# Kernel optimization log

Hardware: AMD Instinct MI355X
Metric: run time of the kernel (lower is better)

The kernel has to match this reference:

```python
import jax, jax.numpy as jnp
import numpy as np

VOCAB, EMBD, H1, H2, OUT = 100000, 128, 256, 128, 1
EPS = 1e-12

def _layernorm(x, g, b):
    mu = jnp.mean(x, axis=-1, keepdims=True)
    var = jnp.mean(jnp.square(x - mu), axis=-1, keepdims=True)
    return (x - mu) * jax.lax.rsqrt(var + EPS) * g + b

def setup_inputs() -> dict:
    key = jax.random.key(0)
    ks = jax.random.split(key, 10)
    B, S = 4096, 50
    return {
        "entity_ids": jax.random.randint(ks[0], (B, S), 0, VOCAB),
        "entity_length": jax.random.randint(ks[1], (B,), 0, S + 1),
        "emb_table": jax.random.normal(ks[2], (VOCAB, EMBD), jnp.float32),
        "ln1_g": jnp.ones((EMBD,), jnp.float32),
        "ln1_b": jnp.zeros((EMBD,), jnp.float32),
        "w1": jax.random.normal(ks[3], (EMBD, H1), jnp.float32) * (1.0 / np.sqrt(EMBD)),
        "b1": jnp.zeros((H1,), jnp.float32),
        "w2": jax.random.normal(ks[4], (H1, H2), jnp.float32) * (1.0 / np.sqrt(H1)),
        "b2": jnp.zeros((H2,), jnp.float32),
        "ln2_g": jnp.ones((H2,), jnp.float32),
        "ln2_b": jnp.zeros((H2,), jnp.float32),
        "fc_w": jax.random.normal(ks[5], (H2, OUT), jnp.float32) * (1.0 / np.sqrt(H2)),
        "fc_b": jnp.zeros((OUT,), jnp.float32),
    }

def reference(entity_ids, entity_length, emb_table, ln1_g, ln1_b, w1, b1, w2, b2, ln2_g, ln2_b, fc_w, fc_b):
    # embed: [B, S, EMBD]
    x = emb_table[entity_ids]
    x = _layernorm(x, ln1_g, ln1_b)
    # MLP (dropout is identity in eval); torch GELU default is exact erf form
    x = jax.nn.gelu(x @ w1 + b1, approximate=False) @ w2 + b2  # [B, S, H2]
    # ragged max-pool over first length positions (length 0 treated as 1)
    lengths = jnp.maximum(entity_length, 1)  # [B]
    S = x.shape[1]
    mask = jnp.arange(S)[None, :] < lengths[:, None]  # [B, S]
    x = jnp.max(jnp.where(mask[:, :, None], x, -jnp.inf), axis=1)  # [B, H2]
    x = _layernorm(x, ln2_g, ln2_b)
    return (x @ fc_w + fc_b).squeeze(-1)  # [B]
```

## Files before the change

kernel.cpp:

```cpp
#include <hip/hip_runtime.h>
#include <hip/hip_bf16.h>
#include <math.h>

typedef __attribute__((ext_vector_type(8))) _Float16 half8;
typedef __attribute__((ext_vector_type(4))) _Float16 half4;
typedef __attribute__((ext_vector_type(4))) float f32x4;

#define EMBD 128
#define H1 256
#define H2 128
#define SLEN 50
#define NROWS 4096
#define MTILE 32
#define DENSE_GRID 256

#define WS_FRAGS   0
#define WS_CNT     131072
#define WS_PACKED  131200
#define WS_PARTIAL 950400

__device__ __forceinline__ float gelu_exact(float h) {
    float ah = fabsf(h);
    float d  = fmaf(0.23163845f, ah, 1.0f);
    float t;
    asm("v_rcp_f32 %0, %1" : "=v"(t) : "v"(d));
    float p = fmaf(1.061405429f, t, -1.453152027f);
    p = fmaf(p, t, 1.421413741f);
    p = fmaf(p, t, -0.284496736f);
    p = fmaf(p, t, 0.254829592f);
    p = p * t;
    float e;
    float x2 = h * h * -0.72134752f;
    asm("v_exp_f32 %0, %1" : "=v"(e) : "v"(x2));
    float er = fmaf(-p, e, 1.0f);
    return fmaf(0.5f * ah, er, 0.5f * h);
}

#define BARRIER_LDS() asm volatile("s_waitcnt lgkmcnt(0)\n\ts_barrier" ::: "memory")

__global__ __launch_bounds__(256) void prep_kernel(
    const float* __restrict__ w1, const float* __restrict__ w2,
    half8* __restrict__ frags, int* __restrict__ cnt,
    float* __restrict__ partial)
{
    int b = blockIdx.x, t = threadIdx.x;
    if (b < 32) {
        int f = b * 256 + t;
        half8 v;
        if (f < 4096) {
            int fragid = f >> 6, lane = f & 63;
            int kt = fragid >> 4, nt = fragid & 15;
            int col = nt * 16 + (lane & 15);
            int kb  = kt * 32 + (lane >> 4) * 8;
            #pragma unroll
            for (int i = 0; i < 8; ++i) v[i] = (_Float16)w1[(size_t)(kb + i) * H1 + col];
            frags[f] = v;
        } else {
            int f2 = f - 4096;
            int fragid = f2 >> 6, lane = f2 & 63;
            int kt = fragid >> 3, ntc = fragid & 7;
            int col = ntc * 16 + (lane & 15);
            int kb  = kt * 32 + (lane >> 4) * 8;
            #pragma unroll
            for (int i = 0; i < 8; ++i) v[i] = (_Float16)w2[(size_t)(kb + i) * H2 + col];
            frags[4096 + f2] = v;
        }
    } else if (b == 32) {
        if (t == 0) *cnt = 0;
    } else {
        int idx = (b - 33) * 256 + t;
        if (idx < NROWS * 256) {
            int r = idx >> 8, rem = idx & 255;
            partial[(size_t)r * 384 + 128 + rem] = -INFINITY;
        }
    }
}

__global__ __launch_bounds__(256) void compact_kernel(
    const int* __restrict__ ids, const int* __restrict__ lens,
    unsigned* __restrict__ packed, int* __restrict__ cnt)
{
    int gtid = blockIdx.x * 256 + threadIdx.x;
    int lane = threadIdx.x & 63;
    int len = lens[gtid]; len = len < 1 ? 1 : (len > SLEN ? SLEN : len);
    int inc = len;
    #pragma unroll
    for (int off = 1; off < 64; off <<= 1) {
        int v = __shfl_up(inc, off, 64);
        if (lane >= off) inc += v;
    }
    int wave_total = __shfl(inc, 63, 64);
    int wbase;
    if (lane == 0) wbase = atomicAdd(cnt, wave_total);
    wbase = __shfl(wbase, 0, 64);
    int base = wbase + inc - len;
    unsigned rtag = (unsigned)gtid << 17;
    for (int t = 0; t < len; ++t)
        packed[base + t] = (unsigned)ids[gtid * SLEN + t] | rtag;
}

__global__ __launch_bounds__(512) void dense_kernel(
    const unsigned* __restrict__ packed, const int* __restrict__ cnt,
    const float* __restrict__ emb, const float* __restrict__ ln1g,
    const float* __restrict__ ln1b, const float* __restrict__ b1,
    const float* __restrict__ b2, const half8* __restrict__ wfrag,
    float* __restrict__ partial)
{
    const int tid = threadIdx.x;
    const int w  = tid >> 6;
    const int l  = tid & 63;
    const int ln = l & 15;
    const int lg = l >> 4;
    const int g32 = w * 4 + lg;

    __shared__ __align__(16) half8 wlds[8192];
    __shared__ __align__(16) _Float16 x_lds[MTILE][EMBD + 8];
    __shared__ __align__(16) _Float16 h1_lds[MTILE][H1 + 8];
    __shared__ unsigned tok_lds[MTILE + 1];

    #pragma unroll
    for (int i = 0; i < 16; ++i)
        wlds[i * 512 + tid] = wfrag[i * 512 + tid];

    float g1r[8], b1r[8];
    #pragma unroll
    for (int i = 0; i < 8; ++i) { g1r[i] = ln1g[ln * 8 + i]; b1r[i] = ln1b[ln * 8 + i]; }
    f32x4 b1tv[2];
    #pragma unroll
    for (int j = 0; j < 2; ++j)
        b1tv[j] = *(const f32x4*)&b1[(w * 2 + j) * 16 + lg * 4];
    const float b2s = b2[w * 16 + ln];

    const int total = *cnt;

    int tile = blockIdx.x;
    int base = tile * MTILE;

    unsigned pkA = 0xFFFFFFFFu, tokA = 0xFFFFFFFFu;
    float4 pa0, pa1; bool vA = false;
    if (base < total) {
        if (base + g32 < total) pkA = packed[base + g32];
        if (tid <= 32) {
            int ti = (tid < 32) ? base + tid : base - 1;
            tokA = (ti >= 0 && ti < total) ? packed[ti] : 0xFFFFFFFFu;
        }
        vA = (pkA != 0xFFFFFFFFu);
        if (vA) {
            int id = (int)(pkA & 0x1FFFFu);
            const float4* src = (const float4*)(emb + (size_t)id * EMBD + ln * 8);
            pa0 = src[0]; pa1 = src[1];
        }
    }

    for (; base < total; tile += (int)gridDim.x, base = tile * MTILE) {
        const int nbase = (tile + (int)gridDim.x) * MTILE;

        if (tid <= 32) tok_lds[tid] = tokA;

        unsigned pkN = 0xFFFFFFFFu, tokN = 0xFFFFFFFFu;
        if (nbase < total) {
            if (nbase + g32 < total) pkN = packed[nbase + g32];
            if (tid <= 32) {
                int ti = (tid < 32) ? nbase + tid : nbase - 1;
                tokN = (ti < total) ? packed[ti] : 0xFFFFFFFFu;
            }
        }

        {
            half8 xo;
            if (vA) {
                float v[8] = {pa0.x, pa0.y, pa0.z, pa0.w, pa1.x, pa1.y, pa1.z, pa1.w};
                float sm = 0.f, ss = 0.f;
                #pragma unroll
                for (int k = 0; k < 8; ++k) { sm += v[k]; ss += v[k] * v[k]; }
                #pragma unroll
                for (int m = 1; m < 16; m <<= 1) {
                    sm += __shfl_xor(sm, m, 64);
                    ss += __shfl_xor(ss, m, 64);
                }
                float mu  = sm * (1.f / 128.f);
                float var = ss * (1.f / 128.f) - mu * mu;
                float rs  = rsqrtf(var + 1e-12f);
                #pragma unroll
                for (int k = 0; k < 8; ++k)
                    xo[k] = (_Float16)((v[k] - mu) * rs * g1r[k] + b1r[k]);
            } else {
                #pragma unroll
                for (int k = 0; k < 8; ++k) xo[k] = (_Float16)0.f;
            }
            *(half8*)&x_lds[g32][ln * 8] = xo;
        }

        BARRIER_LDS();

        f32x4 acc[2][2];
        acc[0][0] = (f32x4){0,0,0,0}; acc[0][1] = (f32x4){0,0,0,0};
        acc[1][0] = (f32x4){0,0,0,0}; acc[1][1] = (f32x4){0,0,0,0};
        #pragma unroll
        for (int kt = 0; kt < 4; ++kt) {
            half8 xf0 = *(const half8*)&x_lds[ln][kt * 32 + lg * 8];
            half8 xf1 = *(const half8*)&x_lds[16 + ln][kt * 32 + lg * 8];
            half8 wf0 = wlds[(kt * 16 + w * 2 + 0) * 64 + l];
            half8 wf1 = wlds[(kt * 16 + w * 2 + 1) * 64 + l];
            acc[0][0] = __builtin_amdgcn_mfma_f32_16x16x32_f16(wf0, xf0, acc[0][0], 0, 0, 0);
            acc[0][1] = __builtin_amdgcn_mfma_f32_16x16x32_f16(wf1, xf0, acc[0][1], 0, 0, 0);
            acc[1][0] = __builtin_amdgcn_mfma_f32_16x16x32_f16(wf0, xf1, acc[1][0], 0, 0, 0);
            acc[1][1] = __builtin_amdgcn_mfma_f32_16x16x32_f16(wf1, xf1, acc[1][1], 0, 0, 0);
        }

        float4 pb0, pb1; bool vN = (pkN != 0xFFFFFFFFu);
        if (vN) {
            int id = (int)(pkN & 0x1FFFFu);
            const float4* src = (const float4*)(emb + (size_t)id * EMBD + ln * 8);
            pb0 = src[0]; pb1 = src[1];
        }

        #pragma unroll
        for (int m = 0; m < 2; ++m)
          #pragma unroll
          for (int j = 0; j < 2; ++j) {
            half4 hv;
            #pragma unroll
            for (int g2 = 0; g2 < 4; ++g2) {
                float h = acc[m][j][g2] + b1tv[j][g2];
                hv[g2] = (_Float16)gelu_exact(h);
            }
            *(half4*)&h1_lds[m * 16 + ln][(w * 2 + j) * 16 + lg * 4] = hv;
          }

        int rowj = 0x7FFF, rowp = 0x7FFF;
        if (l < 32) {
            rowj = (int)(tok_lds[l] >> 17);
            rowp = (l == 0) ? (int)(tok_lds[32] >> 17) : (int)(tok_lds[l - 1] >> 17);
        }
        const int prevrow = (int)(tok_lds[32] >> 17);
        bool st = (l < 32) && ((l == 0) || (rowj != rowp));
        unsigned mask = (unsigned)__ballot(st);

        BARRIER_LDS();

        f32x4 acc2[2];
        acc2[0] = (f32x4){0,0,0,0}; acc2[1] = (f32x4){0,0,0,0};
        #pragma unroll
        for (int kt = 0; kt < 8; ++kt) {
            half8 a0 = *(const half8*)&h1_lds[ln][kt * 32 + lg * 8];
            half8 a1 = *(const half8*)&h1_lds[16 + ln][kt * 32 + lg * 8];
            half8 wf = wlds[4096 + (kt * 8 + w) * 64 + l];
            acc2[0] = __builtin_amdgcn_mfma_f32_16x16x32_f16(a0, wf, acc2[0], 0, 0, 0);
            acc2[1] = __builtin_amdgcn_mfma_f32_16x16x32_f16(a1, wf, acc2[1], 0, 0, 0);
        }
        float val[2][4];
        #pragma unroll
        for (int m = 0; m < 2; ++m)
          #pragma unroll
          for (int g2 = 0; g2 < 4; ++g2)
            val[m][g2] = acc2[m][g2] + b2s;

        {
            int s0 = 0;
            while (s0 < 32) {
                int s1;
                if (s0 >= 31) s1 = 32;
                else {
                    unsigned m2 = mask >> (s0 + 1);
                    s1 = m2 ? (s0 + __ffs(m2)) : 32;
                }
                int row = __shfl(rowj, s0, 64);
                if (row < NROWS) {
                    float mx = -INFINITY;
                    #pragma unroll
                    for (int m = 0; m < 2; ++m)
                      #pragma unroll
                      for (int g2 = 0; g2 < 4; ++g2) {
                        int tt = m * 16 + lg * 4 + g2;
                        if (tt >= s0 && tt < s1) mx = fmaxf(mx, val[m][g2]);
                      }
                    mx = fmaxf(mx, __shfl_xor(mx, 16, 64));
                    mx = fmaxf(mx, __shfl_xor(mx, 32, 64));
                    int side = (s0 == 0 && row == prevrow) ? 1 + (tile & 1) : 0;
                    if (l < 16)
                        partial[(size_t)row * 384 + side * 128 + w * 16 + l] = mx;
                }
                s0 = s1;
            }
        }

        pkA = pkN; tokA = tokN; vA = vN;
        if (vN) { pa0 = pb0; pa1 = pb1; }
    }
}

__global__ __launch_bounds__(256) void head_kernel(
    const float* __restrict__ partial, const float* __restrict__ ln2g,
    const float* __restrict__ ln2b, const float* __restrict__ fcw,
    const float* __restrict__ fcb, float* __restrict__ out)
{
    int w = threadIdx.x >> 6, l = threadIdx.x & 63;
    int r = blockIdx.x * 4 + w;
    const float* pr = partial + (size_t)r * 384;
    float v0 = fmaxf(fmaxf(pr[l],      pr[128 + l]),      pr[256 + l]);
    float v1 = fmaxf(fmaxf(pr[64 + l], pr[128 + 64 + l]), pr[256 + 64 + l]);
    float g2a = ln2g[l], g2c = ln2g[l + 64];
    float b2a = ln2b[l], b2c = ln2b[l + 64];
    float fwa = fcw[l],  fwc = fcw[l + 64];
    float s = v0 + v1, ss = v0 * v0 + v1 * v1;
    #pragma unroll
    for (int m = 1; m < 64; m <<= 1) {
        s  += __shfl_xor(s,  m, 64);
        ss += __shfl_xor(ss, m, 64);
    }
    float mu  = s * (1.f / 128.f);
    float var = ss * (1.f / 128.f) - mu * mu;
    float rs  = rsqrtf(var + 1e-12f);
    float n0 = (v0 - mu) * rs * g2a + b2a;
    float n1 = (v1 - mu) * rs * g2c + b2c;
    float dot = n0 * fwa + n1 * fwc;
    #pragma unroll
    for (int m = 1; m < 64; m <<= 1) dot += __shfl_xor(dot, m, 64);
    if (l == 0) out[r] = dot + fcb[0];
}

extern "C" void kernel_launch(void* const* d_in, const int* in_sizes, int n_in,
                              void* d_out, int out_size, void* d_ws, size_t ws_size,
                              hipStream_t stream) {
    const int*   ids  = (const int*)d_in[0];
    const int*   lens = (const int*)d_in[1];
    const float* emb  = (const float*)d_in[2];
    const float* ln1g = (const float*)d_in[3];
    const float* ln1b = (const float*)d_in[4];
    const float* w1   = (const float*)d_in[5];
    const float* b1   = (const float*)d_in[6];
    const float* w2   = (const float*)d_in[7];
    const float* b2   = (const float*)d_in[8];
    const float* ln2g = (const float*)d_in[9];
    const float* ln2b = (const float*)d_in[10];
    const float* fcw  = (const float*)d_in[11];
    const float* fcb  = (const float*)d_in[12];
    float* out = (float*)d_out;

    char* ws = (char*)d_ws;
    half8*    frags   = (half8*)(ws + WS_FRAGS);
    int*      cnt     = (int*)(ws + WS_CNT);
    unsigned* packed  = (unsigned*)(ws + WS_PACKED);
    float*    partial = (float*)(ws + WS_PARTIAL);

    hipLaunchKernelGGL(prep_kernel, dim3(4129), dim3(256), 0, stream,
                       w1, w2, frags, cnt, partial);
    hipLaunchKernelGGL(compact_kernel, dim3(16), dim3(256), 0, stream,
                       ids, lens, packed, cnt);
    hipLaunchKernelGGL(dense_kernel, dim3(DENSE_GRID), dim3(512), 0, stream,
                       packed, cnt, emb, ln1g, ln1b, b1, b2, frags, partial);
    hipLaunchKernelGGL(head_kernel, dim3(1024), dim3(256), 0, stream,
                       partial, ln2g, ln2b, fcw, fcb, out);
}
```

Measured before the change: 70.42 us.

## Hold MLP weight fragments in registers, merge prep kernels, double dense grid

Removes the 128KB weight staging buffer from LDS. Each wave now keeps its own W1/W2 MFMA fragments in VGPRs, which lowers LDS use so more dense blocks can be resident per CU, and the dense grid doubles from 256 to 512 blocks. The compaction kernel is folded into the prep kernel, the counter reset becomes a hipMemsetAsync, and the -inf fill of the partial buffer uses float4 stores in a grid-stride loop. The risk is higher register pressure from 16 half8 weight fragments per lane, and every block re-reading the weights from global memory.

```diff
diff --git a/kernel.cpp b/kernel.cpp
--- a/kernel.cpp
+++ b/kernel.cpp
@@ -12,7 +12,7 @@
 #define SLEN 50
 #define NROWS 4096
 #define MTILE 32
-#define DENSE_GRID 256
+#define DENSE_GRID 512
 
 #define WS_FRAGS   0
 #define WS_CNT     131072
@@ -38,10 +38,11 @@
 
 #define BARRIER_LDS() asm volatile("s_waitcnt lgkmcnt(0)\n\ts_barrier" ::: "memory")
 
-__global__ __launch_bounds__(256) void prep_kernel(
+__global__ __launch_bounds__(256) void setup_kernel(
     const float* __restrict__ w1, const float* __restrict__ w2,
-    half8* __restrict__ frags, int* __restrict__ cnt,
-    float* __restrict__ partial)
+    const int* __restrict__ ids, const int* __restrict__ lens,
+    half8* __restrict__ frags, unsigned* __restrict__ packed,
+    int* __restrict__ cnt, float* __restrict__ partial)
 {
     int b = blockIdx.x, t = threadIdx.x;
     if (b < 32) {
@@ -65,38 +66,33 @@
             for (int i = 0; i < 8; ++i) v[i] = (_Float16)w2[(size_t)(kb + i) * H2 + col];
             frags[4096 + f2] = v;
         }
-    } else if (b == 32) {
-        if (t == 0) *cnt = 0;
+    } else if (b < 48) {
+        int gtid = (b - 32) * 256 + t;
+        int lane = t & 63;
+        int len = lens[gtid]; len = len < 1 ? 1 : (len > SLEN ? SLEN : len);
+        int inc = len;
+        #pragma unroll
+        for (int off = 1; off < 64; off <<= 1) {
+            int v = __shfl_up(inc, off, 64);
+            if (lane >= off) inc += v;
+        }
+        int wave_total = __shfl(inc, 63, 64);
+        int wbase;
+        if (lane == 0) wbase = atomicAdd(cnt, wave_total);
+        wbase = __shfl(wbase, 0, 64);
+        int base = wbase + inc - len;
+        unsigned rtag = (unsigned)gtid << 17;
+        for (int k = 0; k < len; ++k)
+            packed[base + k] = (unsigned)ids[gtid * SLEN + k] | rtag;
     } else {
-        int idx = (b - 33) * 256 + t;
-        if (idx < NROWS * 256) {
-            int r = idx >> 8, rem = idx & 255;
-            partial[(size_t)r * 384 + 128 + rem] = -INFINITY;
+        float4 ninf = { -INFINITY, -INFINITY, -INFINITY, -INFINITY };
+        float4* p4 = (float4*)partial;
+        int idx = (b - 48) * 256 + t;
+        for (int e = idx; e < NROWS * 64; e += 64 * 256) {
+            int row = e >> 6, rem = e & 63;
+            p4[row * 96 + 32 + rem] = ninf;
         }
     }
-}
-
-__global__ __launch_bounds__(256) void compact_kernel(
-    const int* __restrict__ ids, const int* __restrict__ lens,
-    unsigned* __restrict__ packed, int* __restrict__ cnt)
-{
-    int gtid = blockIdx.x * 256 + threadIdx.x;
-    int lane = threadIdx.x & 63;
-    int len = lens[gtid]; len = len < 1 ? 1 : (len > SLEN ? SLEN : len);
-    int inc = len;
-    #pragma unroll
-    for (int off = 1; off < 64; off <<= 1) {
-        int v = __shfl_up(inc, off, 64);
-        if (lane >= off) inc += v;
-    }
-    int wave_total = __shfl(inc, 63, 64);
-    int wbase;
-    if (lane == 0) wbase = atomicAdd(cnt, wave_total);
-    wbase = __shfl(wbase, 0, 64);
-    int base = wbase + inc - len;
-    unsigned rtag = (unsigned)gtid << 17;
-    for (int t = 0; t < len; ++t)
-        packed[base + t] = (unsigned)ids[gtid * SLEN + t] | rtag;
 }
 
 __global__ __launch_bounds__(512) void dense_kernel(
@@ -113,23 +109,29 @@
     const int lg = l >> 4;
     const int g32 = w * 4 + lg;
 
-    __shared__ __align__(16) half8 wlds[8192];
     __shared__ __align__(16) _Float16 x_lds[MTILE][EMBD + 8];
     __shared__ __align__(16) _Float16 h1_lds[MTILE][H1 + 8];
     __shared__ unsigned tok_lds[MTILE + 1];
-
-    #pragma unroll
-    for (int i = 0; i < 16; ++i)
-        wlds[i * 512 + tid] = wfrag[i * 512 + tid];
+    __shared__ __align__(16) float b1s[H1];
+    __shared__ float b2s[H2];
+
+    if (tid < H1) b1s[tid] = b1[tid];
+    else if (tid < H1 + H2) b2s[tid - H1] = b2[tid - H1];
+
+    half8 w1r[4][2];
+    #pragma unroll
+    for (int kt = 0; kt < 4; ++kt)
+      #pragma unroll
+      for (int j = 0; j < 2; ++j)
+        w1r[kt][j] = wfrag[(kt * 16 + w * 2 + j) * 64 + l];
+    half8 w2r[8];
+    #pragma unroll
+    for (int kt = 0; kt < 8; ++kt)
+        w2r[kt] = wfrag[4096 + (kt * 8 + w) * 64 + l];
 
     float g1r[8], b1r[8];
     #pragma unroll
     for (int i = 0; i < 8; ++i) { g1r[i] = ln1g[ln * 8 + i]; b1r[i] = ln1b[ln * 8 + i]; }
-    f32x4 b1tv[2];
-    #pragma unroll
-    for (int j = 0; j < 2; ++j)
-        b1tv[j] = *(const f32x4*)&b1[(w * 2 + j) * 16 + lg * 4];
-    const float b2s = b2[w * 16 + ln];
 
     const int total = *cnt;
 
@@ -146,8 +148,7 @@
         }
         vA = (pkA != 0xFFFFFFFFu);
         if (vA) {
-            int id = (int)(pkA & 0x1FFFFu);
-            const float4* src = (const float4*)(emb + (size_t)id * EMBD + ln * 8);
+            const float4* src = (const float4*)(emb + (size_t)(pkA & 0x1FFFFu) * EMBD + ln * 8);
             pa0 = src[0]; pa1 = src[1];
         }
     }
@@ -200,18 +201,15 @@
         for (int kt = 0; kt < 4; ++kt) {
             half8 xf0 = *(const half8*)&x_lds[ln][kt * 32 + lg * 8];
             half8 xf1 = *(const half8*)&x_lds[16 + ln][kt * 32 + lg * 8];
-            half8 wf0 = wlds[(kt * 16 + w * 2 + 0) * 64 + l];
-            half8 wf1 = wlds[(kt * 16 + w * 2 + 1) * 64 + l];
-            acc[0][0] = __builtin_amdgcn_mfma_f32_16x16x32_f16(wf0, xf0, acc[0][0], 0, 0, 0);
-            acc[0][1] = __builtin_amdgcn_mfma_f32_16x16x32_f16(wf1, xf0, acc[0][1], 0, 0, 0);
-            acc[1][0] = __builtin_amdgcn_mfma_f32_16x16x32_f16(wf0, xf1, acc[1][0], 0, 0, 0);
-            acc[1][1] = __builtin_amdgcn_mfma_f32_16x16x32_f16(wf1, xf1, acc[1][1], 0, 0, 0);
+            acc[0][0] = __builtin_amdgcn_mfma_f32_16x16x32_f16(w1r[kt][0], xf0, acc[0][0], 0, 0, 0);
+            acc[0][1] = __builtin_amdgcn_mfma_f32_16x16x32_f16(w1r[kt][1], xf0, acc[0][1], 0, 0, 0);
+            acc[1][0] = __builtin_amdgcn_mfma_f32_16x16x32_f16(w1r[kt][0], xf1, acc[1][0], 0, 0, 0);
+            acc[1][1] = __builtin_amdgcn_mfma_f32_16x16x32_f16(w1r[kt][1], xf1, acc[1][1], 0, 0, 0);
         }
 
         float4 pb0, pb1; bool vN = (pkN != 0xFFFFFFFFu);
         if (vN) {
-            int id = (int)(pkN & 0x1FFFFu);
-            const float4* src = (const float4*)(emb + (size_t)id * EMBD + ln * 8);
+            const float4* src = (const float4*)(emb + (size_t)(pkN & 0x1FFFFu) * EMBD + ln * 8);
             pb0 = src[0]; pb1 = src[1];
         }
 
@@ -219,10 +217,11 @@
         for (int m = 0; m < 2; ++m)
           #pragma unroll
           for (int j = 0; j < 2; ++j) {
+            f32x4 bb = *(const f32x4*)&b1s[(w * 2 + j) * 16 + lg * 4];
             half4 hv;
             #pragma unroll
             for (int g2 = 0; g2 < 4; ++g2) {
-                float h = acc[m][j][g2] + b1tv[j][g2];
+                float h = acc[m][j][g2] + bb[g2];
                 hv[g2] = (_Float16)gelu_exact(h);
             }
             *(half4*)&h1_lds[m * 16 + ln][(w * 2 + j) * 16 + lg * 4] = hv;
@@ -236,6 +235,7 @@
         const int prevrow = (int)(tok_lds[32] >> 17);
         bool st = (l < 32) && ((l == 0) || (rowj != rowp));
         unsigned mask = (unsigned)__ballot(st);
+        const float b2v = b2s[w * 16 + ln];
 
         BARRIER_LDS();
 
@@ -245,16 +245,15 @@
         for (int kt = 0; kt < 8; ++kt) {
             half8 a0 = *(const half8*)&h1_lds[ln][kt * 32 + lg * 8];
             half8 a1 = *(const half8*)&h1_lds[16 + ln][kt * 32 + lg * 8];
-            half8 wf = wlds[4096 + (kt * 8 + w) * 64 + l];
-            acc2[0] = __builtin_amdgcn_mfma_f32_16x16x32_f16(a0, wf, acc2[0], 0, 0, 0);
-            acc2[1] = __builtin_amdgcn_mfma_f32_16x16x32_f16(a1, wf, acc2[1], 0, 0, 0);
+            acc2[0] = __builtin_amdgcn_mfma_f32_16x16x32_f16(a0, w2r[kt], acc2[0], 0, 0, 0);
+            acc2[1] = __builtin_amdgcn_mfma_f32_16x16x32_f16(a1, w2r[kt], acc2[1], 0, 0, 0);
         }
         float val[2][4];
         #pragma unroll
         for (int m = 0; m < 2; ++m)
           #pragma unroll
           for (int g2 = 0; g2 < 4; ++g2)
-            val[m][g2] = acc2[m][g2] + b2s;
+            val[m][g2] = acc2[m][g2] + b2v;
 
         {
             int s0 = 0;
@@ -344,10 +343,9 @@
     unsigned* packed  = (unsigned*)(ws + WS_PACKED);
     float*    partial = (float*)(ws + WS_PARTIAL);
 
-    hipLaunchKernelGGL(prep_kernel, dim3(4129), dim3(256), 0, stream,
-                       w1, w2, frags, cnt, partial);
-    hipLaunchKernelGGL(compact_kernel, dim3(16), dim3(256), 0, stream,
-                       ids, lens, packed, cnt);
+    hipMemsetAsync(cnt, 0, sizeof(int), stream);
+    hipLaunchKernelGGL(setup_kernel, dim3(112), dim3(256), 0, stream,
+                       w1, w2, ids, lens, frags, packed, cnt, partial);
     hipLaunchKernelGGL(dense_kernel, dim3(DENSE_GRID), dim3(512), 0, stream,
                        packed, cnt, emb, ln1g, ln1b, b1, b2, frags, partial);
     hipLaunchKernelGGL(head_kernel, dim3(1024), dim3(256), 0, stream,
```

After: 72.58 us. 3.1% more time.
